# Kernel tuning notes

Hardware: AMD Instinct MI355X
Metric: run time of the kernel (lower is better)

The kernel has to match this reference:

```python
import jax, jax.numpy as jnp
import numpy as np

B, Q, K = 8, 128, 1024
QK_DIM = 512   # query_size == key_size
HID = 256      # hidden_size
VDIM = 512     # value feature dim
NEG = -1e6     # mask fill value used by the torch code


def setup_inputs() -> dict:
    key = jax.random.key(0)
    ks = jax.random.split(key, 7)
    queries = jax.random.normal(ks[0], (B, Q, QK_DIM), dtype=jnp.float32)
    keys = jax.random.normal(ks[1], (B, K, QK_DIM), dtype=jnp.float32)
    values = jax.random.normal(ks[2], (B, K, VDIM), dtype=jnp.float32)
    valid_lens = jax.random.randint(ks[3], (B,), 1, K + 1, dtype=jnp.int32)
    # Linear weights (no bias); scaled like torch default init
    Wq = jax.random.normal(ks[4], (QK_DIM, HID), dtype=jnp.float32) / np.sqrt(QK_DIM)
    Wk = jax.random.normal(ks[5], (QK_DIM, HID), dtype=jnp.float32) / np.sqrt(QK_DIM)
    wv = jax.random.normal(ks[6], (HID,), dtype=jnp.float32) / np.sqrt(HID)
    return {"queries": queries, "keys": keys, "values": values,
            "valid_lens": valid_lens, "Wq": Wq, "Wk": Wk, "wv": wv}


def reference(queries, keys, values, valid_lens, Wq, Wk, wv):
    q = jnp.einsum('bqd,dh->bqh', queries, Wq)          # [B,Q,H]
    k = jnp.einsum('bkd,dh->bkh', keys, Wk)             # [B,K,H]
    # broadcast add -> tanh -> score projection
    features = jnp.tanh(q[:, :, None, :] + k[:, None, :, :])  # [B,Q,K,H]
    scores = jnp.einsum('bqkh,h->bqk', features, wv)    # [B,Q,K]
    # masked softmax over last axis (valid_lens per batch row)
    mask = jnp.arange(scores.shape[-1])[None, None, :] < valid_lens[:, None, None]
    scores = jnp.where(mask, scores, NEG)
    attn = jax.nn.softmax(scores, axis=-1)              # [B,Q,K]
    # dropout is identity in eval mode (p=0)
    return jnp.einsum('bqk,bkv->bqv', attn, values)     # [B,Q,VDIM]
```

## Files before the change

### kernel.cpp

```cpp
#include <hip/hip_runtime.h>
#include <math.h>

#define NB 8
#define NQ 128
#define NK 1024
#define ND 512
#define NH 256
#define NV 512

typedef __attribute__((ext_vector_type(8))) short short8v;
typedef __attribute__((ext_vector_type(4))) float floatx4;


__device__ __forceinline__ ushort f2bf(float f) {
  union { float f; unsigned u; } v; v.f = f;
  unsigned r = (v.u + 0x7FFF + ((v.u >> 16) & 1)) >> 16;
  return (ushort)r;
}
__device__ __forceinline__ float bf2f(ushort b) {
  union { unsigned u; float f; } v; v.u = ((unsigned)b) << 16;
  return v.f;
}
__device__ __forceinline__ float wave_rsum(float v) {
#pragma unroll
  for (int off = 32; off; off >>= 1) v += __shfl_xor(v, off);
  return v;
}

__global__ __launch_bounds__(64) void splitw_kernel(
    const float* __restrict__ Wq, const float* __restrict__ Wk,
    ushort* __restrict__ WpQ, ushort* __restrict__ WpK,
    float* __restrict__ rowsum) {
  const int l = threadIdx.x;
  const int blk = blockIdx.x;
  if (blockIdx.y == 0 && blk < 16) rowsum[blk * 64 + l] = 0.f;
  const float* W = blockIdx.y ? Wk : Wq;
  ushort* O = blockIdx.y ? WpK : WpQ;
  const int col = ((blk >> 4) << 4) + (l & 15);
  const int dbase = (blk & 15) * 32 + ((l >> 4) << 3);
  ushort h8[8], l8[8];
#pragma unroll
  for (int j = 0; j < 8; ++j) {
    float f = W[(size_t)(dbase + j) * NH + col];
    ushort hi = f2bf(f);
    h8[j] = hi;
    l8[j] = f2bf(f - bf2f(hi));
  }
  ushort* oh = &O[(size_t)blk * 1024 + l * 8];
  *(ushort4*)&oh[0] = make_ushort4(h8[0], h8[1], h8[2], h8[3]);
  *(ushort4*)&oh[4] = make_ushort4(h8[4], h8[5], h8[6], h8[7]);
  *(ushort4*)&oh[512] = make_ushort4(l8[0], l8[1], l8[2], l8[3]);
  *(ushort4*)&oh[516] = make_ushort4(l8[4], l8[5], l8[6], l8[7]);
}

__global__ __launch_bounds__(256) void convert_v_kernel(
    const float* __restrict__ values, const int* __restrict__ valid_lens,
    ushort* __restrict__ Vp) {
  const int b = blockIdx.z;
  const int k0 = blockIdx.x * 32;
  const int v0 = blockIdx.y * 32;
  const int V = valid_lens[b];
  if (k0 >= ((V + 31) & ~31)) return;
  const int t = threadIdx.x;
  __shared__ float tile[32][33];
#pragma unroll
  for (int i = 0; i < 4; ++i) {
    int idx = t + 256 * i;
    int kk = idx >> 5, vv = idx & 31;
    tile[kk][vv] = values[(size_t)(b * NK + k0 + kk) * NV + v0 + vv];
  }
  __syncthreads();
  const int vv = t & 31, k4 = t >> 5;
  const int kr = k4 * 4;
  const size_t base = ((size_t)(b * 32 + ((v0 + vv) >> 4)) * 32 + (k0 >> 5)) * 512;
  const int off = ((vv & 15) << 3) + (((kr >> 3) & 3) << 7) + (kr & 7);
  ushort4 o;
  o.x = f2bf(tile[kr + 0][vv]);
  o.y = f2bf(tile[kr + 1][vv]);
  o.z = f2bf(tile[kr + 2][vv]);
  o.w = f2bf(tile[kr + 3][vv]);
  *(ushort4*)&Vp[base + off] = o;
}

__global__ __launch_bounds__(256, 1) void proj_mfma_kernel(
    const float* __restrict__ queries, const float* __restrict__ keys,
    const ushort* __restrict__ WpQ, const ushort* __restrict__ WpK,
    const int* __restrict__ valid_lens,
    float* __restrict__ Eq, ushort* __restrict__ EkTb) {
  const int t = threadIdx.x;
  const int lane = t & 63, wvid = t >> 6;
  const int lr = lane & 15, lg = lane >> 4;
  const int bx = blockIdx.x;
  const bool isQ = bx < 64;
  const float* A;
  const ushort* Wp;
  int arow0, b = 0, rin = 0;
  if (isQ) {
    A = queries; Wp = WpQ; arow0 = bx * 16;
  } else {
    int kt = bx - 64;
    b = kt >> 6; rin = (kt & 63) * 16;
    if (rin >= valid_lens[b]) return;
    A = keys; Wp = WpK; arow0 = b * NK + rin;
  }

  __shared__ ushort Wlds[3][4][8][512];
  __shared__ ushort Ah[16][520];
  __shared__ ushort Al[16][520];

#define ISSUE(buf, kkv)                                                        \
  {                                                                            \
    _Pragma("unroll") for (int f = 0; f < 8; ++f) {                            \
      const ushort* g = &Wp[((size_t)((wvid * 4 + (f >> 1)) * 16 + (kkv))      \
                             << 10) + ((f & 1) << 9) + lane * 8];              \
      __builtin_amdgcn_global_load_lds(                                        \
          (const __attribute__((address_space(1))) void*)g,                    \
          (__attribute__((address_space(3))) void*)&Wlds[buf][wvid][f][0],     \
          16, 0, 0);                                                           \
    }                                                                          \
  }

  ISSUE(0, 0);
  ISSUE(1, 1);

  {
    const float* Arow = A + (size_t)arow0 * ND;
#pragma unroll
    for (int i = 0; i < 8; ++i) {
      int e = (t + 256 * i) * 4;
      int r = e >> 9, c = e & 511;
      float4 a = *(const float4*)&Arow[e];
      ushort4 h, l;
      h.x = f2bf(a.x); l.x = f2bf(a.x - bf2f(h.x));
      h.y = f2bf(a.y); l.y = f2bf(a.y - bf2f(h.y));
      h.z = f2bf(a.z); l.z = f2bf(a.z - bf2f(h.z));
      h.w = f2bf(a.w); l.w = f2bf(a.w - bf2f(h.w));
      *(ushort4*)&Ah[r][c] = h;
      *(ushort4*)&Al[r][c] = l;
    }
  }
  __syncthreads();

  floatx4 acc[4];
#pragma unroll
  for (int c = 0; c < 4; ++c) acc[c] = (floatx4){0.f, 0.f, 0.f, 0.f};

#pragma unroll
  for (int kk = 0; kk < 16; ++kk) {
    if (kk + 2 < 16) ISSUE((kk + 2) % 3, kk + 2);
    if (kk < 14)      asm volatile("s_waitcnt vmcnt(16)" ::: "memory");
    else if (kk == 14) asm volatile("s_waitcnt vmcnt(8)" ::: "memory");
    else               asm volatile("s_waitcnt vmcnt(0)" ::: "memory");
    const short8v ah_ = *(const short8v*)&Ah[lr][kk * 32 + lg * 8];
    const short8v al_ = *(const short8v*)&Al[lr][kk * 32 + lg * 8];
#pragma unroll
    for (int c = 0; c < 4; ++c) {
      const short8v wh_ = *(const short8v*)&Wlds[kk % 3][wvid][c * 2 + 0][lane * 8];
      const short8v wl_ = *(const short8v*)&Wlds[kk % 3][wvid][c * 2 + 1][lane * 8];
      acc[c] = __builtin_amdgcn_mfma_f32_16x16x32_bf16(al_, wh_, acc[c], 0, 0, 0);
      acc[c] = __builtin_amdgcn_mfma_f32_16x16x32_bf16(ah_, wl_, acc[c], 0, 0, 0);
      acc[c] = __builtin_amdgcn_mfma_f32_16x16x32_bf16(ah_, wh_, acc[c], 0, 0, 0);
    }
  }
#undef ISSUE

  const float C2 = 2.885390081777927f;
  if (isQ) {
#pragma unroll
    for (int c = 0; c < 4; ++c) {
      const int h = wvid * 64 + c * 16 + lr;
#pragma unroll
      for (int reg = 0; reg < 4; ++reg) {
        const int row = arow0 + lg * 4 + reg;
        float p = fminf(fmaxf(acc[c][reg], -15.f), 15.f);
        Eq[(size_t)row * NH + h] = exp2f(p * C2);
      }
    }
  } else {
#pragma unroll
    for (int c = 0; c < 4; ++c) {
      const int h = wvid * 64 + c * 16 + lr;
      ushort4 e;
      e.x = f2bf(exp2f(fminf(fmaxf(acc[c][0], -15.f), 15.f) * C2));
      e.y = f2bf(exp2f(fminf(fmaxf(acc[c][1], -15.f), 15.f) * C2));
      e.z = f2bf(exp2f(fminf(fmaxf(acc[c][2], -15.f), 15.f) * C2));
      e.w = f2bf(exp2f(fminf(fmaxf(acc[c][3], -15.f), 15.f) * C2));
      *(ushort4*)&EkTb[((size_t)(b * NH + h)) * NK + rin + lg * 4] = e;
    }
  }
}

__global__ __launch_bounds__(256, 2) void score_kernel(
    const float* __restrict__ Eq, const ushort* __restrict__ EkTb,
    const float* __restrict__ wvp, const int* __restrict__ valid_lens,
    ushort* __restrict__ Pbp, float* __restrict__ rowsum) {
  const int b = blockIdx.z;
  const int V = valid_lens[b];
  const int k0 = blockIdx.y * 256;
  if (k0 >= V) return;
  const int t = threadIdx.x;
  const int q0 = blockIdx.x * 4;
  const int lane = t & 63, wid = t >> 6;
  const float L2E2 = 2.8853900817779268f;

  __shared__ __align__(16) float eqs[4][NH];
  __shared__ __align__(16) float wvs[NH];
  __shared__ float red[20];

  ((float4*)eqs)[t] = ((const float4*)&Eq[(size_t)(b * NQ + q0) * NH])[t];
  wvs[t] = wvp[t];
  __syncthreads();

  float mn = wave_rsum(fminf(wvs[t], 0.f));
  if (lane == 0) red[wid] = mn;
  __syncthreads();
  const float SN = -(red[0] + red[1] + red[2] + red[3]);

  const ushort* ek = EkTb + (size_t)b * NH * NK + k0 + t;
  float a0 = 0.f, a1 = 0.f, a2 = 0.f, a3 = 0.f;

  ushort uA[8], uB[8];
#define LOADE(u, h0)                                                      \
  {                                                                       \
    _Pragma("unroll") for (int j = 0; j < 8; ++j)                         \
        u[j] = ek[(size_t)((h0) + j) * NK];                               \
  }
#define CHUNK(u, h0)                                                      \
  {                                                                       \
    float e0[8], e1[8], e2[8], e3[8], w8[8];                              \
    *(float4*)&e0[0] = *(const float4*)&eqs[0][(h0)];                     \
    *(float4*)&e0[4] = *(const float4*)&eqs[0][(h0) + 4];                 \
    *(float4*)&e1[0] = *(const float4*)&eqs[1][(h0)];                     \
    *(float4*)&e1[4] = *(const float4*)&eqs[1][(h0) + 4];                 \
    *(float4*)&e2[0] = *(const float4*)&eqs[2][(h0)];                     \
    *(float4*)&e2[4] = *(const float4*)&eqs[2][(h0) + 4];                 \
    *(float4*)&e3[0] = *(const float4*)&eqs[3][(h0)];                     \
    *(float4*)&e3[4] = *(const float4*)&eqs[3][(h0) + 4];                 \
    *(float4*)&w8[0] = *(const float4*)&wvs[(h0)];                        \
    *(float4*)&w8[4] = *(const float4*)&wvs[(h0) + 4];                    \
    _Pragma("unroll") for (int j = 0; j < 8; ++j) {                       \
      const float ev = bf2f(u[j]);                                        \
      a0 += w8[j] * __builtin_amdgcn_rcpf(__builtin_fmaf(e0[j], ev, 1.f)); \
      a1 += w8[j] * __builtin_amdgcn_rcpf(__builtin_fmaf(e1[j], ev, 1.f)); \
      a2 += w8[j] * __builtin_amdgcn_rcpf(__builtin_fmaf(e2[j], ev, 1.f)); \
      a3 += w8[j] * __builtin_amdgcn_rcpf(__builtin_fmaf(e3[j], ev, 1.f)); \
    }                                                                     \
  }

  LOADE(uA, 0);
#pragma unroll 1
  for (int h0 = 0; h0 < NH; h0 += 16) {
    LOADE(uB, h0 + 8);
    CHUNK(uA, h0);
    if (h0 + 16 < NH) LOADE(uA, h0 + 16);
    CHUNK(uB, h0 + 8);
  }
#undef LOADE
#undef CHUNK

  const int k = k0 + t;
  const bool ok = (k < V);
  float p[4];
  p[0] = ok ? exp2f(-L2E2 * (a0 + SN)) : 0.f;
  p[1] = ok ? exp2f(-L2E2 * (a1 + SN)) : 0.f;
  p[2] = ok ? exp2f(-L2E2 * (a2 + SN)) : 0.f;
  p[3] = ok ? exp2f(-L2E2 * (a3 + SN)) : 0.f;

  const size_t blk0 = ((size_t)(b * 8 + (q0 >> 4)) * 32 + (k0 >> 5) + (t >> 5)) * 512;
  const int offk = (((t >> 3) & 3) << 7) + (t & 7);
#pragma unroll
  for (int i = 0; i < 4; ++i) {
    const ushort ui = f2bf(p[i]);
    Pbp[blk0 + (((q0 + i) & 15) << 3) + offk] = ui;
    float s = wave_rsum(bf2f(ui));
    if (lane == 0) red[4 + i * 4 + wid] = s;
  }
  __syncthreads();
  if (t < 4)
    atomicAdd(&rowsum[b * NQ + q0 + t],
              red[4 + t * 4] + red[5 + t * 4] + red[6 + t * 4] + red[7 + t * 4]);
}

__global__ __launch_bounds__(128, 2) void pv_mfma_kernel(
    const ushort* __restrict__ Pbp, const ushort* __restrict__ Vp,
    const float* __restrict__ rowsum, const int* __restrict__ valid_lens,
    float* __restrict__ out) {
  const int w = threadIdx.x >> 6;
  const int lane = threadIdx.x & 63;
  const int lr = lane & 15, lg = lane >> 4;
  const int qt = blockIdx.x, vt2 = blockIdx.y, b = blockIdx.z;
  const int V = valid_lens[b];
  const int Kt4 = (((V + 31) >> 5) + 3) & ~3;
  const int vt = vt2 * 2 + w;
  const ushort* pbase = Pbp + ((size_t)(b * 8 + qt) * 32) * 512 + lane * 8;
  const ushort* vbase = Vp + ((size_t)(b * 32 + vt) * 32) * 512 + lane * 8;

#define LP(s) (*(const short8v*)&pbase[(size_t)(s) * 512])
#define LV(s) (*(const short8v*)&vbase[(size_t)(s) * 512])

  floatx4 acc0 = (floatx4){0.f, 0.f, 0.f, 0.f};
  floatx4 acc1 = (floatx4){0.f, 0.f, 0.f, 0.f};
  short8v pA, vA, pB, vB, pC, vC, pD, vD;
  pA = LP(0); vA = LV(0);
  pB = LP(1); vB = LV(1);
  pC = LP(2); vC = LV(2);
  for (int s = 0; s < Kt4; s += 4) {
    pD = LP(s + 3); vD = LV(s + 3);
    acc0 = __builtin_amdgcn_mfma_f32_16x16x32_bf16(pA, vA, acc0, 0, 0, 0);
    if (s + 4 < Kt4) { pA = LP(s + 4); vA = LV(s + 4); }
    acc1 = __builtin_amdgcn_mfma_f32_16x16x32_bf16(pB, vB, acc1, 0, 0, 0);
    if (s + 5 < Kt4) { pB = LP(s + 5); vB = LV(s + 5); }
    acc0 = __builtin_amdgcn_mfma_f32_16x16x32_bf16(pC, vC, acc0, 0, 0, 0);
    if (s + 6 < Kt4) { pC = LP(s + 6); vC = LV(s + 6); }
    acc1 = __builtin_amdgcn_mfma_f32_16x16x32_bf16(pD, vD, acc1, 0, 0, 0);
  }
#undef LP
#undef LV

#pragma unroll
  for (int reg = 0; reg < 4; ++reg) {
    const int row = b * NQ + qt * 16 + lg * 4 + reg;
    const float rs = __builtin_amdgcn_rcpf(rowsum[row]);
    out[(size_t)row * NV + vt * 16 + lr] = (acc0[reg] + acc1[reg]) * rs;
  }
}

extern "C" void kernel_launch(void* const* d_in, const int* in_sizes, int n_in,
                              void* d_out, int out_size, void* d_ws, size_t ws_size,
                              hipStream_t stream) {
  const float* queries = (const float*)d_in[0];
  const float* keys    = (const float*)d_in[1];
  const float* values  = (const float*)d_in[2];
  const int*   vlens   = (const int*)d_in[3];
  const float* Wq      = (const float*)d_in[4];
  const float* Wk      = (const float*)d_in[5];
  const float* wv      = (const float*)d_in[6];
  float* out = (float*)d_out;

  char* base = (char*)d_ws;
  ushort* WpQ  = (ushort*)base;
  ushort* WpK  = WpQ + 256 * 1024;
  float*  Eq   = (float*)(base + (1 << 20));
  ushort* EkTb = (ushort*)(base + (2 << 20));
  ushort* Pbp  = (ushort*)(base + (6 << 20));
  ushort* Vp   = (ushort*)(base + (8 << 20));
  float*  rowsum = (float*)(base + (16 << 20));

  splitw_kernel<<<dim3(256, 2), dim3(64), 0, stream>>>(Wq, Wk, WpQ, WpK, rowsum);
  convert_v_kernel<<<dim3(32, 16, 8), dim3(256), 0, stream>>>(values, vlens, Vp);
  proj_mfma_kernel<<<dim3(576), dim3(256), 0, stream>>>(
      queries, keys, WpQ, WpK, vlens, Eq, EkTb);
  score_kernel<<<dim3(32, 4, 8), dim3(256), 0, stream>>>(
      Eq, EkTb, wv, vlens, Pbp, rowsum);
  pv_mfma_kernel<<<dim3(8, 16, 8), dim3(128), 0, stream>>>(
      Pbp, Vp, rowsum, vlens, out);
}
```

Measured before the change: 150.5 us.

## Merge prep kernels and pre-split A operands into bf16 fragment layout for projection

Folds the weight split, V conversion and rowsum zeroing into one prep kernel, which also converts queries and keys into hi/lo bf16 fragment-ordered tiles. The projection kernel becomes a single-wave block computing a 32-row by 64-column tile, streaming both A and W fragments through a double-buffered global-to-LDS pipeline. This removes one launch and the per-block fp32 A conversion in the projection, at the cost of an extra global round trip for the split A operands and more, smaller blocks.

Measured after the change: 148.7 us. No clear change (-1.2%).

```diff
diff --git a/kernel.cpp b/kernel.cpp
--- a/kernel.cpp
+++ b/kernel.cpp
@@ -27,140 +27,174 @@
   return v;
 }
 
-__global__ __launch_bounds__(64) void splitw_kernel(
+__global__ __launch_bounds__(256) void prep_kernel(
+    const float* __restrict__ q, const float* __restrict__ kys,
+    const float* __restrict__ vals, const int* __restrict__ vl,
     const float* __restrict__ Wq, const float* __restrict__ Wk,
     ushort* __restrict__ WpQ, ushort* __restrict__ WpK,
+    ushort* __restrict__ Ap, ushort* __restrict__ Vp,
     float* __restrict__ rowsum) {
-  const int l = threadIdx.x;
-  const int blk = blockIdx.x;
-  if (blockIdx.y == 0 && blk < 16) rowsum[blk * 64 + l] = 0.f;
-  const float* W = blockIdx.y ? Wk : Wq;
-  ushort* O = blockIdx.y ? WpK : WpQ;
-  const int col = ((blk >> 4) << 4) + (l & 15);
-  const int dbase = (blk & 15) * 32 + ((l >> 4) << 3);
-  ushort h8[8], l8[8];
-#pragma unroll
-  for (int j = 0; j < 8; ++j) {
-    float f = W[(size_t)(dbase + j) * NH + col];
-    ushort hi = f2bf(f);
-    h8[j] = hi;
-    l8[j] = f2bf(f - bf2f(hi));
-  }
-  ushort* oh = &O[(size_t)blk * 1024 + l * 8];
-  *(ushort4*)&oh[0] = make_ushort4(h8[0], h8[1], h8[2], h8[3]);
-  *(ushort4*)&oh[4] = make_ushort4(h8[4], h8[5], h8[6], h8[7]);
-  *(ushort4*)&oh[512] = make_ushort4(l8[0], l8[1], l8[2], l8[3]);
-  *(ushort4*)&oh[516] = make_ushort4(l8[4], l8[5], l8[6], l8[7]);
-}
-
-__global__ __launch_bounds__(256) void convert_v_kernel(
-    const float* __restrict__ values, const int* __restrict__ valid_lens,
-    ushort* __restrict__ Vp) {
-  const int b = blockIdx.z;
-  const int k0 = blockIdx.x * 32;
-  const int v0 = blockIdx.y * 32;
-  const int V = valid_lens[b];
-  if (k0 >= ((V + 31) & ~31)) return;
-  const int t = threadIdx.x;
-  __shared__ float tile[32][33];
-#pragma unroll
-  for (int i = 0; i < 4; ++i) {
-    int idx = t + 256 * i;
-    int kk = idx >> 5, vv = idx & 31;
-    tile[kk][vv] = values[(size_t)(b * NK + k0 + kk) * NV + v0 + vv];
-  }
-  __syncthreads();
-  const int vv = t & 31, k4 = t >> 5;
-  const int kr = k4 * 4;
-  const size_t base = ((size_t)(b * 32 + ((v0 + vv) >> 4)) * 32 + (k0 >> 5)) * 512;
-  const int off = ((vv & 15) << 3) + (((kr >> 3) & 3) << 7) + (kr & 7);
-  ushort4 o;
-  o.x = f2bf(tile[kr + 0][vv]);
-  o.y = f2bf(tile[kr + 1][vv]);
-  o.z = f2bf(tile[kr + 2][vv]);
-  o.w = f2bf(tile[kr + 3][vv]);
-  *(ushort4*)&Vp[base + off] = o;
-}
-
-__global__ __launch_bounds__(256, 1) void proj_mfma_kernel(
-    const float* __restrict__ queries, const float* __restrict__ keys,
+  const int bi = blockIdx.x, t = threadIdx.x;
+  if (bi < 128) {
+    const int unit = (bi << 2) | (t >> 6);
+    const int mat = unit >> 8, blk = unit & 255, l = t & 63;
+    const float* W = mat ? Wk : Wq;
+    ushort* O = mat ? WpK : WpQ;
+    const int col = ((blk >> 4) << 4) + (l & 15);
+    const int dbase = (blk & 15) * 32 + ((l >> 4) << 3);
+    ushort h8[8], l8[8];
+#pragma unroll
+    for (int j = 0; j < 8; ++j) {
+      float f = W[(size_t)(dbase + j) * NH + col];
+      ushort hi = f2bf(f);
+      h8[j] = hi;
+      l8[j] = f2bf(f - bf2f(hi));
+    }
+    ushort* oh = &O[(size_t)blk * 1024 + l * 8];
+    *(ushort4*)&oh[0] = make_ushort4(h8[0], h8[1], h8[2], h8[3]);
+    *(ushort4*)&oh[4] = make_ushort4(h8[4], h8[5], h8[6], h8[7]);
+    *(ushort4*)&oh[512] = make_ushort4(l8[0], l8[1], l8[2], l8[3]);
+    *(ushort4*)&oh[516] = make_ushort4(l8[4], l8[5], l8[6], l8[7]);
+  } else if (bi < 2432) {
+    const int bi2 = bi - 128;
+    const int rg = bi2 >> 4, kk = bi2 & 15;
+    const int r0 = rg * 64;
+    const float* src;
+    int srow;
+    if (r0 < 1024) { src = q; srow = r0; }
+    else {
+      const int rk = r0 - 1024;
+      const int b = rk >> 10, rin = rk & 1023;
+      if (rin >= vl[b]) return;
+      src = kys; srow = rk;
+    }
+    const int row = t >> 2, dq = t & 3;
+    const float* p = &src[(size_t)(srow + row) * ND + kk * 32 + dq * 8];
+    const float4 a0 = *(const float4*)p;
+    const float4 a1 = *(const float4*)(p + 4);
+    ushort4 h0, l0, h1, l1;
+    h0.x = f2bf(a0.x); l0.x = f2bf(a0.x - bf2f(h0.x));
+    h0.y = f2bf(a0.y); l0.y = f2bf(a0.y - bf2f(h0.y));
+    h0.z = f2bf(a0.z); l0.z = f2bf(a0.z - bf2f(h0.z));
+    h0.w = f2bf(a0.w); l0.w = f2bf(a0.w - bf2f(h0.w));
+    h1.x = f2bf(a1.x); l1.x = f2bf(a1.x - bf2f(h1.x));
+    h1.y = f2bf(a1.y); l1.y = f2bf(a1.y - bf2f(h1.y));
+    h1.z = f2bf(a1.z); l1.z = f2bf(a1.z - bf2f(h1.z));
+    h1.w = f2bf(a1.w); l1.w = f2bf(a1.w - bf2f(h1.w));
+    const size_t blkidx = ((size_t)((r0 + row) >> 4) * 16 + kk) * 1024;
+    const int lp = ((row & 15) | (dq << 4)) * 8;
+    *(ushort4*)&Ap[blkidx + lp] = h0;
+    *(ushort4*)&Ap[blkidx + lp + 4] = h1;
+    *(ushort4*)&Ap[blkidx + 512 + lp] = l0;
+    *(ushort4*)&Ap[blkidx + 512 + lp + 4] = l1;
+  } else if (bi < 6528) {
+    const int bi3 = bi - 2432;
+    const int b = bi3 >> 9, rest = bi3 & 511;
+    const int k0 = (rest >> 4) * 32, v0 = (rest & 15) * 32;
+    const int V = vl[b];
+    if (k0 >= ((V + 31) & ~31)) return;
+    __shared__ float tile[32][33];
+#pragma unroll
+    for (int i = 0; i < 4; ++i) {
+      int idx = t + 256 * i;
+      int kk = idx >> 5, vv = idx & 31;
+      tile[kk][vv] = vals[(size_t)(b * NK + k0 + kk) * NV + v0 + vv];
+    }
+    __syncthreads();
+    const int vv = t & 31, kr = (t >> 5) * 4;
+    const size_t base = ((size_t)(b * 32 + ((v0 + vv) >> 4)) * 32 + (k0 >> 5)) * 512;
+    const int off = ((vv & 15) << 3) + (((kr >> 3) & 3) << 7) + (kr & 7);
+    ushort4 o;
+    o.x = f2bf(tile[kr + 0][vv]);
+    o.y = f2bf(tile[kr + 1][vv]);
+    o.z = f2bf(tile[kr + 2][vv]);
+    o.w = f2bf(tile[kr + 3][vv]);
+    *(ushort4*)&Vp[base + off] = o;
+  } else {
+    for (int i = t; i < NB * NQ; i += 256) rowsum[i] = 0.f;
+  }
+}
+
+__global__ __launch_bounds__(64, 2) void proj_mfma_kernel(
     const ushort* __restrict__ WpQ, const ushort* __restrict__ WpK,
-    const int* __restrict__ valid_lens,
+    const ushort* __restrict__ Ap, const int* __restrict__ vl,
     float* __restrict__ Eq, ushort* __restrict__ EkTb) {
-  const int t = threadIdx.x;
-  const int lane = t & 63, wvid = t >> 6;
+  const int lane = threadIdx.x;
   const int lr = lane & 15, lg = lane >> 4;
   const int bx = blockIdx.x;
-  const bool isQ = bx < 64;
-  const float* A;
+  const int rp = bx >> 2, cg = bx & 3;
+  const int r0 = rp * 32;
+  const bool isQ = r0 < 1024;
   const ushort* Wp;
-  int arow0, b = 0, rin = 0;
+  int b = 0, rin = 0;
   if (isQ) {
-    A = queries; Wp = WpQ; arow0 = bx * 16;
+    Wp = WpQ;
   } else {
-    int kt = bx - 64;
-    b = kt >> 6; rin = (kt & 63) * 16;
-    if (rin >= valid_lens[b]) return;
-    A = keys; Wp = WpK; arow0 = b * NK + rin;
-  }
-
-  __shared__ ushort Wlds[3][4][8][512];
-  __shared__ ushort Ah[16][520];
-  __shared__ ushort Al[16][520];
-
-#define ISSUE(buf, kkv)                                                        \
+    const int rk = r0 - 1024;
+    b = rk >> 10; rin = rk & 1023;
+    if (rin >= vl[b]) return;
+    Wp = WpK;
+  }
+  const int fb0 = r0 >> 4;
+
+  __shared__ ushort Wr[2][4][2][512];
+  __shared__ ushort Ar[2][2][2][512];
+
+#define ISSUE(slot, kkv)                                                       \
   {                                                                            \
-    _Pragma("unroll") for (int f = 0; f < 8; ++f) {                            \
-      const ushort* g = &Wp[((size_t)((wvid * 4 + (f >> 1)) * 16 + (kkv))      \
-                             << 10) + ((f & 1) << 9) + lane * 8];              \
-      __builtin_amdgcn_global_load_lds(                                        \
-          (const __attribute__((address_space(1))) void*)g,                    \
-          (__attribute__((address_space(3))) void*)&Wlds[buf][wvid][f][0],     \
-          16, 0, 0);                                                           \
+    _Pragma("unroll") for (int cf = 0; cf < 4; ++cf) {                         \
+      _Pragma("unroll") for (int hf = 0; hf < 2; ++hf) {                       \
+        const ushort* g = &Wp[(((size_t)(cg * 4 + cf) * 16 + (kkv)) << 10) +   \
+                              (hf << 9) + lane * 8];                           \
+        __builtin_amdgcn_global_load_lds(                                      \
+            (const __attribute__((address_space(1))) void*)g,                  \
+            (__attribute__((address_space(3))) void*)&Wr[slot][cf][hf][0],     \
+            16, 0, 0);                                                         \
+      }                                                                        \
+    }                                                                          \
+    _Pragma("unroll") for (int rf = 0; rf < 2; ++rf) {                         \
+      _Pragma("unroll") for (int hf = 0; hf < 2; ++hf) {                       \
+        const ushort* g = &Ap[(((size_t)(fb0 + rf) * 16 + (kkv)) << 10) +      \
+                              (hf << 9) + lane * 8];                           \
+        __builtin_amdgcn_global_load_lds(                                      \
+            (const __attribute__((address_space(1))) void*)g,                  \
+            (__attribute__((address_space(3))) void*)&Ar[slot][rf][hf][0],     \
+            16, 0, 0);                                                         \
+      }                                                                        \
     }                                                                          \
   }
 
   ISSUE(0, 0);
   ISSUE(1, 1);
 
-  {
-    const float* Arow = A + (size_t)arow0 * ND;
-#pragma unroll
-    for (int i = 0; i < 8; ++i) {
-      int e = (t + 256 * i) * 4;
-      int r = e >> 9, c = e & 511;
-      float4 a = *(const float4*)&Arow[e];
-      ushort4 h, l;
-      h.x = f2bf(a.x); l.x = f2bf(a.x - bf2f(h.x));
-      h.y = f2bf(a.y); l.y = f2bf(a.y - bf2f(h.y));
-      h.z = f2bf(a.z); l.z = f2bf(a.z - bf2f(h.z));
-      h.w = f2bf(a.w); l.w = f2bf(a.w - bf2f(h.w));
-      *(ushort4*)&Ah[r][c] = h;
-      *(ushort4*)&Al[r][c] = l;
-    }
-  }
-  __syncthreads();
-
-  floatx4 acc[4];
-#pragma unroll
-  for (int c = 0; c < 4; ++c) acc[c] = (floatx4){0.f, 0.f, 0.f, 0.f};
+  floatx4 acc0[4], acc1[4];
+#pragma unroll
+  for (int c = 0; c < 4; ++c) {
+    acc0[c] = (floatx4){0.f, 0.f, 0.f, 0.f};
+    acc1[c] = (floatx4){0.f, 0.f, 0.f, 0.f};
+  }
 
 #pragma unroll
   for (int kk = 0; kk < 16; ++kk) {
-    if (kk + 2 < 16) ISSUE((kk + 2) % 3, kk + 2);
-    if (kk < 14)      asm volatile("s_waitcnt vmcnt(16)" ::: "memory");
-    else if (kk == 14) asm volatile("s_waitcnt vmcnt(8)" ::: "memory");
-    else               asm volatile("s_waitcnt vmcnt(0)" ::: "memory");
-    const short8v ah_ = *(const short8v*)&Ah[lr][kk * 32 + lg * 8];
-    const short8v al_ = *(const short8v*)&Al[lr][kk * 32 + lg * 8];
+    const int sl = kk & 1;
+    if (kk < 15) asm volatile("s_waitcnt vmcnt(12)" ::: "memory");
+    else         asm volatile("s_waitcnt vmcnt(0)" ::: "memory");
+    const short8v ah0 = *(const short8v*)&Ar[sl][0][0][lane * 8];
+    const short8v al0 = *(const short8v*)&Ar[sl][0][1][lane * 8];
+    const short8v ah1 = *(const short8v*)&Ar[sl][1][0][lane * 8];
+    const short8v al1 = *(const short8v*)&Ar[sl][1][1][lane * 8];
 #pragma unroll
     for (int c = 0; c < 4; ++c) {
-      const short8v wh_ = *(const short8v*)&Wlds[kk % 3][wvid][c * 2 + 0][lane * 8];
-      const short8v wl_ = *(const short8v*)&Wlds[kk % 3][wvid][c * 2 + 1][lane * 8];
-      acc[c] = __builtin_amdgcn_mfma_f32_16x16x32_bf16(al_, wh_, acc[c], 0, 0, 0);
-      acc[c] = __builtin_amdgcn_mfma_f32_16x16x32_bf16(ah_, wl_, acc[c], 0, 0, 0);
-      acc[c] = __builtin_amdgcn_mfma_f32_16x16x32_bf16(ah_, wh_, acc[c], 0, 0, 0);
-    }
+      const short8v wh = *(const short8v*)&Wr[sl][c][0][lane * 8];
+      const short8v wl = *(const short8v*)&Wr[sl][c][1][lane * 8];
+      acc0[c] = __builtin_amdgcn_mfma_f32_16x16x32_bf16(al0, wh, acc0[c], 0, 0, 0);
+      acc0[c] = __builtin_amdgcn_mfma_f32_16x16x32_bf16(ah0, wl, acc0[c], 0, 0, 0);
+      acc0[c] = __builtin_amdgcn_mfma_f32_16x16x32_bf16(ah0, wh, acc0[c], 0, 0, 0);
+      acc1[c] = __builtin_amdgcn_mfma_f32_16x16x32_bf16(al1, wh, acc1[c], 0, 0, 0);
+      acc1[c] = __builtin_amdgcn_mfma_f32_16x16x32_bf16(ah1, wl, acc1[c], 0, 0, 0);
+      acc1[c] = __builtin_amdgcn_mfma_f32_16x16x32_bf16(ah1, wh, acc1[c], 0, 0, 0);
+    }
+    if (kk < 14) ISSUE(sl, kk + 2);
   }
 #undef ISSUE
 
@@ -168,24 +202,31 @@
   if (isQ) {
 #pragma unroll
     for (int c = 0; c < 4; ++c) {
-      const int h = wvid * 64 + c * 16 + lr;
+      const int h = cg * 64 + c * 16 + lr;
 #pragma unroll
       for (int reg = 0; reg < 4; ++reg) {
-        const int row = arow0 + lg * 4 + reg;
-        float p = fminf(fmaxf(acc[c][reg], -15.f), 15.f);
-        Eq[(size_t)row * NH + h] = exp2f(p * C2);
+        const int row0 = r0 + lg * 4 + reg;
+        float p0 = fminf(fmaxf(acc0[c][reg], -15.f), 15.f);
+        float p1 = fminf(fmaxf(acc1[c][reg], -15.f), 15.f);
+        Eq[(size_t)row0 * NH + h] = exp2f(p0 * C2);
+        Eq[(size_t)(row0 + 16) * NH + h] = exp2f(p1 * C2);
       }
     }
   } else {
 #pragma unroll
     for (int c = 0; c < 4; ++c) {
-      const int h = wvid * 64 + c * 16 + lr;
-      ushort4 e;
-      e.x = f2bf(exp2f(fminf(fmaxf(acc[c][0], -15.f), 15.f) * C2));
-      e.y = f2bf(exp2f(fminf(fmaxf(acc[c][1], -15.f), 15.f) * C2));
-      e.z = f2bf(exp2f(fminf(fmaxf(acc[c][2], -15.f), 15.f) * C2));
-      e.w = f2bf(exp2f(fminf(fmaxf(acc[c][3], -15.f), 15.f) * C2));
-      *(ushort4*)&EkTb[((size_t)(b * NH + h)) * NK + rin + lg * 4] = e;
+      const int h = cg * 64 + c * 16 + lr;
+      ushort4 e0, e1;
+      e0.x = f2bf(exp2f(fminf(fmaxf(acc0[c][0], -15.f), 15.f) * C2));
+      e0.y = f2bf(exp2f(fminf(fmaxf(acc0[c][1], -15.f), 15.f) * C2));
+      e0.z = f2bf(exp2f(fminf(fmaxf(acc0[c][2], -15.f), 15.f) * C2));
+      e0.w = f2bf(exp2f(fminf(fmaxf(acc0[c][3], -15.f), 15.f) * C2));
+      e1.x = f2bf(exp2f(fminf(fmaxf(acc1[c][0], -15.f), 15.f) * C2));
+      e1.y = f2bf(exp2f(fminf(fmaxf(acc1[c][1], -15.f), 15.f) * C2));
+      e1.z = f2bf(exp2f(fminf(fmaxf(acc1[c][2], -15.f), 15.f) * C2));
+      e1.w = f2bf(exp2f(fminf(fmaxf(acc1[c][3], -15.f), 15.f) * C2));
+      *(ushort4*)&EkTb[((size_t)(b * NH + h)) * NK + rin + lg * 4] = e0;
+      *(ushort4*)&EkTb[((size_t)(b * NH + h)) * NK + rin + 16 + lg * 4] = e1;
     }
   }
 }
@@ -345,11 +386,12 @@
   ushort* Pbp  = (ushort*)(base + (6 << 20));
   ushort* Vp   = (ushort*)(base + (8 << 20));
   float*  rowsum = (float*)(base + (16 << 20));
-
-  splitw_kernel<<<dim3(256, 2), dim3(64), 0, stream>>>(Wq, Wk, WpQ, WpK, rowsum);
-  convert_v_kernel<<<dim3(32, 16, 8), dim3(256), 0, stream>>>(values, vlens, Vp);
-  proj_mfma_kernel<<<dim3(576), dim3(256), 0, stream>>>(
-      queries, keys, WpQ, WpK, vlens, Eq, EkTb);
+  ushort* Ap   = (ushort*)(base + (17 << 20));
+
+  prep_kernel<<<dim3(6529), dim3(256), 0, stream>>>(
+      queries, keys, values, vlens, Wq, Wk, WpQ, WpK, Ap, Vp, rowsum);
+  proj_mfma_kernel<<<dim3(1152), dim3(64), 0, stream>>>(
+      WpQ, WpK, Ap, vlens, Eq, EkTb);
   score_kernel<<<dim3(32, 4, 8), dim3(256), 0, stream>>>(
       Eq, EkTb, wv, vlens, Pbp, rowsum);
   pv_mfma_kernel<<<dim3(8, 16, 8), dim3(128), 0, stream>>>(
```
